# Kernel optimization log

Hardware: AMD Instinct MI355X
Metric: run time of the kernel (lower is better)

The kernel has to match this reference:

```python
import jax, jax.numpy as jnp
import numpy as np

H = 8
D_MODEL = 512
D_K = D_MODEL // H


def setup_inputs() -> dict:
    key = jax.random.key(0)
    ks = jax.random.split(key, 12)
    B, S = 4, 2048
    scale = 1.0 / np.sqrt(D_MODEL)
    inp = {
        "query": jax.random.normal(ks[0], (B, S, D_MODEL), jnp.float32),
        "key": jax.random.normal(ks[1], (B, S, D_MODEL), jnp.float32),
        "value": jax.random.normal(ks[2], (B, S, D_MODEL), jnp.float32),
        "mask": jnp.ones((B, 1, S), jnp.int32),
        "Wq": jax.random.normal(ks[3], (D_MODEL, D_MODEL), jnp.float32) * scale,
        "bq": jax.random.normal(ks[4], (D_MODEL,), jnp.float32) * 0.01,
        "Wk": jax.random.normal(ks[5], (D_MODEL, D_MODEL), jnp.float32) * scale,
        "bk": jax.random.normal(ks[6], (D_MODEL,), jnp.float32) * 0.01,
        "Wv": jax.random.normal(ks[7], (D_MODEL, D_MODEL), jnp.float32) * scale,
        "bv": jax.random.normal(ks[8], (D_MODEL,), jnp.float32) * 0.01,
        "Wo": jax.random.normal(ks[9], (D_MODEL, D_MODEL), jnp.float32) * scale,
        "bo": jax.random.normal(ks[10], (D_MODEL,), jnp.float32) * 0.01,
    }
    return inp


def reference(query, key, value, mask, Wq, bq, Wk, bk, Wv, bv, Wo, bo):
    B, S, _ = query.shape

    def proj(x, W, b):
        # [B,S,D] -> [B,H,S,d_k]
        y = jnp.einsum('bsd,ed->bse', x, W) + b  # torch Linear: x @ W.T + b
        return y.reshape(B, S, H, D_K).transpose(0, 2, 1, 3)

    q = proj(query, Wq, bq)
    k = proj(key, Wk, bk)
    v = proj(value, Wv, bv)

    scores = jnp.einsum('bhqd,bhkd->bhqk', q, k) / jnp.sqrt(jnp.float32(D_K))
    m = mask[:, None, :, :]  # [B,1,1,S]
    scores = jnp.where(m == 0, jnp.float32(-1e9), scores)
    p_attn = jax.nn.softmax(scores, axis=-1)  # dropout is identity in eval
    x = jnp.einsum('bhqk,bhkd->bhqd', p_attn, v)
    x = x.transpose(0, 2, 1, 3).reshape(B, S, D_MODEL)
    return jnp.einsum('bsd,ed->bse', x, Wo) + bo
```

## Files before the change

### kernel.cpp

```cpp
#include <hip/hip_runtime.h>
#include <hip/hip_bf16.h>

#define H 8
#define DMODEL 512
#define DK 64
#define BATCH 4
#define SEQ 2048
#define M_TOTAL (BATCH*SEQ)

typedef short bf16x8 __attribute__((ext_vector_type(8)));
typedef float f32x4 __attribute__((ext_vector_type(4)));
typedef float f32x16 __attribute__((ext_vector_type(16)));

__device__ __forceinline__ unsigned short f2bf(float f) {
    unsigned int u = __builtin_bit_cast(unsigned int, f);
    u += 0x7FFFu + ((u >> 16) & 1u);
    return (unsigned short)(u >> 16);
}

__device__ __forceinline__ unsigned int pack_bf2(float a, float b) {
    unsigned int r;
    asm("v_cvt_pk_bf16_f32 %0, %1, %2" : "=v"(r) : "v"(a), "v"(b));
    return r;
}

__device__ __forceinline__ float exp2_fast(float x) {
    float r;
    asm("v_exp_f32 %0, %1" : "=v"(r) : "v"(x));
    return r;
}

__device__ __forceinline__ f32x16 zero16() {
    f32x16 z;
    #pragma unroll
    for (int i = 0; i < 16; i++) z[i] = 0.f;
    return z;
}

__global__ __launch_bounds__(256) void gemm_qkv(
    const float* __restrict__ query, const float* __restrict__ key_,
    const float* __restrict__ value,
    const float* __restrict__ Wq, const float* __restrict__ bq,
    const float* __restrict__ Wk, const float* __restrict__ bk,
    const float* __restrict__ Wv, const float* __restrict__ bv,
    unsigned short* __restrict__ Qh, unsigned short* __restrict__ Kh,
    unsigned short* __restrict__ Vt)
{
    const int z = blockIdx.z;
    const float* A    = (z == 0) ? query : (z == 1) ? key_ : value;
    const float* W    = (z == 0) ? Wq : (z == 1) ? Wk : Wv;
    const float* bias = (z == 0) ? bq : (z == 1) ? bk : bv;
    unsigned short* out = (z == 0) ? Qh : (z == 1) ? Kh : Vt;

    const int m0 = blockIdx.x * 128;
    const int n0 = blockIdx.y * 64;
    const int tid = threadIdx.x;
    const int lane = tid & 63;
    const int w = tid >> 6;
    const int g = lane >> 4, qi = lane & 15;
    const int wm = w >> 1, wn = w & 1;

    __shared__ unsigned short Alds[128 * 40];
    __shared__ unsigned short Blds[64 * 40];

    f32x4 acc[4][2];
    #pragma unroll
    for (int i = 0; i < 4; i++)
        #pragma unroll
        for (int j = 0; j < 2; j++) acc[i][j] = f32x4{0.f, 0.f, 0.f, 0.f};

    float4 aA[4], bA[2], aB[4], bB[2];

    auto ld = [&](float4 (&ar)[4], float4 (&br)[2], int k0) {
        #pragma unroll
        for (int i = 0; i < 4; i++) { int idx = tid + i * 256;
            ar[i] = *(const float4*)(A + (size_t)(m0 + (idx >> 3)) * 512 + k0 + (idx & 7) * 4); }
        #pragma unroll
        for (int i = 0; i < 2; i++) { int idx = tid + i * 256;
            br[i] = *(const float4*)(W + (size_t)(n0 + (idx >> 3)) * 512 + k0 + (idx & 7) * 4); }
    };
    auto st = [&](float4 (&ar)[4], float4 (&br)[2]) {
        #pragma unroll
        for (int i = 0; i < 4; i++) { int idx = tid + i * 256;
            uint2 p; p.x = pack_bf2(ar[i].x, ar[i].y); p.y = pack_bf2(ar[i].z, ar[i].w);
            *(uint2*)(Alds + (idx >> 3) * 40 + (idx & 7) * 4) = p; }
        #pragma unroll
        for (int i = 0; i < 2; i++) { int idx = tid + i * 256;
            uint2 p; p.x = pack_bf2(br[i].x, br[i].y); p.y = pack_bf2(br[i].z, br[i].w);
            *(uint2*)(Blds + (idx >> 3) * 40 + (idx & 7) * 4) = p; }
    };
    auto tile = [&]() {
        bf16x8 af[4], bf[2];
        #pragma unroll
        for (int mt = 0; mt < 4; mt++)
            af[mt] = *(const bf16x8*)(Alds + (wm * 64 + mt * 16 + qi) * 40 + g * 8);
        #pragma unroll
        for (int nt = 0; nt < 2; nt++)
            bf[nt] = *(const bf16x8*)(Blds + (wn * 32 + nt * 16 + qi) * 40 + g * 8);
        #pragma unroll
        for (int mt = 0; mt < 4; mt++)
            #pragma unroll
            for (int nt = 0; nt < 2; nt++)
                acc[mt][nt] = __builtin_amdgcn_mfma_f32_16x16x32_bf16(af[mt], bf[nt], acc[mt][nt], 0, 0, 0);
    };

    ld(aA, bA, 0);
    for (int k0 = 0; k0 < 512; k0 += 64) {
        __syncthreads();
        st(aA, bA);
        ld(aB, bB, k0 + 32);
        __syncthreads();
        tile();
        __syncthreads();
        st(aB, bB);
        if (k0 + 64 < 512) ld(aA, bA, k0 + 64);
        __syncthreads();
        tile();
    }

    #pragma unroll
    for (int mt = 0; mt < 4; mt++) {
        int mbase = m0 + wm * 64 + mt * 16 + g * 4;
        #pragma unroll
        for (int nt = 0; nt < 2; nt++) {
            int n = n0 + wn * 32 + nt * 16 + qi;
            float bv = bias[n];
            int h = n >> 6, dk = n & 63;
            if (z == 2) {
                int b = mbase >> 11, s = mbase & 2047;
                uint2 pk;
                pk.x = pack_bf2(acc[mt][nt][0] + bv, acc[mt][nt][1] + bv);
                pk.y = pack_bf2(acc[mt][nt][2] + bv, acc[mt][nt][3] + bv);
                *(uint2*)(out + ((size_t)(b * H + h) * 64 + dk) * SEQ + s) = pk;
            } else {
                float sc = (z == 0) ? 0.18033688011112042f : 1.0f;
                #pragma unroll
                for (int r = 0; r < 4; r++) {
                    int m = mbase + r;
                    int b = m >> 11, s = m & 2047;
                    out[((size_t)(b * H + h) * SEQ + s) * 64 + dk] = f2bf((acc[mt][nt][r] + bv) * sc);
                }
            }
        }
    }
}

__global__ __launch_bounds__(256) void gemm_o(
    const unsigned short* __restrict__ Xa, const float* __restrict__ W,
    const float* __restrict__ bias, float* __restrict__ out)
{
    const int m0 = blockIdx.x * 128;
    const int n0 = blockIdx.y * 64;
    const int tid = threadIdx.x;
    const int lane = tid & 63;
    const int w = tid >> 6;
    const int g = lane >> 4, qi = lane & 15;
    const int wm = w >> 1, wn = w & 1;

    __shared__ unsigned short Alds[128 * 40];
    __shared__ unsigned short Blds[64 * 40];

    f32x4 acc[4][2];
    #pragma unroll
    for (int i = 0; i < 4; i++)
        #pragma unroll
        for (int j = 0; j < 2; j++) acc[i][j] = f32x4{0.f, 0.f, 0.f, 0.f};

    bf16x8 aA[2], aB[2];
    float4 bA[2], bB[2];

    auto ld = [&](bf16x8 (&ar)[2], float4 (&br)[2], int k0) {
        #pragma unroll
        for (int i = 0; i < 2; i++) { int idx = tid + i * 256;
            ar[i] = *(const bf16x8*)(Xa + (size_t)(m0 + (idx >> 2)) * 512 + k0 + (idx & 3) * 8); }
        #pragma unroll
        for (int i = 0; i < 2; i++) { int idx = tid + i * 256;
            br[i] = *(const float4*)(W + (size_t)(n0 + (idx >> 3)) * 512 + k0 + (idx & 7) * 4); }
    };
    auto st = [&](bf16x8 (&ar)[2], float4 (&br)[2]) {
        #pragma unroll
        for (int i = 0; i < 2; i++) { int idx = tid + i * 256;
            *(bf16x8*)(Alds + (idx >> 2) * 40 + (idx & 3) * 8) = ar[i]; }
        #pragma unroll
        for (int i = 0; i < 2; i++) { int idx = tid + i * 256;
            uint2 p; p.x = pack_bf2(br[i].x, br[i].y); p.y = pack_bf2(br[i].z, br[i].w);
            *(uint2*)(Blds + (idx >> 3) * 40 + (idx & 7) * 4) = p; }
    };
    auto tile = [&]() {
        bf16x8 af[4], bf[2];
        #pragma unroll
        for (int mt = 0; mt < 4; mt++)
            af[mt] = *(const bf16x8*)(Alds + (wm * 64 + mt * 16 + qi) * 40 + g * 8);
        #pragma unroll
        for (int nt = 0; nt < 2; nt++)
            bf[nt] = *(const bf16x8*)(Blds + (wn * 32 + nt * 16 + qi) * 40 + g * 8);
        #pragma unroll
        for (int mt = 0; mt < 4; mt++)
            #pragma unroll
            for (int nt = 0; nt < 2; nt++)
                acc[mt][nt] = __builtin_amdgcn_mfma_f32_16x16x32_bf16(af[mt], bf[nt], acc[mt][nt], 0, 0, 0);
    };

    ld(aA, bA, 0);
    for (int k0 = 0; k0 < 512; k0 += 64) {
        __syncthreads();
        st(aA, bA);
        ld(aB, bB, k0 + 32);
        __syncthreads();
        tile();
        __syncthreads();
        st(aB, bB);
        if (k0 + 64 < 512) ld(aA, bA, k0 + 64);
        __syncthreads();
        tile();
    }

    #pragma unroll
    for (int mt = 0; mt < 4; mt++) {
        int mbase = m0 + wm * 64 + mt * 16 + g * 4;
        #pragma unroll
        for (int nt = 0; nt < 2; nt++) {
            int n = n0 + wn * 32 + nt * 16 + qi;
            float bv = bias[n];
            #pragma unroll
            for (int r = 0; r < 4; r++)
                out[(size_t)(mbase + r) * 512 + n] = acc[mt][nt][r] + bv;
        }
    }
}

__global__ __launch_bounds__(256, 2) void attn_kernel(
    const unsigned short* __restrict__ Qh,
    const unsigned short* __restrict__ Kh,
    const unsigned short* __restrict__ Vt,
    const int* __restrict__ mask,
    unsigned short* __restrict__ Xattn)
{
    const int tid = threadIdx.x;
    const int lane = tid & 63;
    const int w = tid >> 6;
    const int c = lane & 31;
    const int hi = lane >> 5;
    const int x7 = lane & 7;

    const int bid = blockIdx.x;
    const int xcd = bid & 7;
    const int slot = bid >> 3;
    const int bh = xcd * 4 + (slot >> 4);
    const int q0 = (slot & 15) * 128;
    const int b = bh >> 3;

    __shared__ unsigned short Klds[3][64 * 64];
    __shared__ unsigned short Vlds[3][64 * 64];
    __shared__ int amflag;

    bf16x8 qfr[4];
    {
        const unsigned short* Qbase =
            Qh + ((size_t)bh * SEQ + q0 + w * 32 + c) * 64 + hi * 8;
        #pragma unroll
        for (int seg = 0; seg < 4; seg++)
            qfr[seg] = *(const bf16x8*)(Qbase + seg * 16);
    }

    f32x16 acc[2];
    acc[0] = zero16();
    acc[1] = zero16();
    float l_lane = 0.f;

    const unsigned char* Kbh = (const unsigned char*)(Kh + (size_t)bh * SEQ * 64);
    const unsigned char* Vbh = (const unsigned char*)(Vt + (size_t)bh * 64 * SEQ);
    const int* maskb = mask + b * SEQ;

    if (tid == 0) amflag = 1;
    __syncthreads();
    {
        int v = 1;
        #pragma unroll
        for (int i = 0; i < 8; i++) v &= (maskb[tid + i * 256] != 0) ? 1 : 0;
        if (__ballot(v != 0) != ~0ull && lane == 0) amflag = 0;
    }
    __syncthreads();
    const bool allmask = (amflag != 0);

    const int klane = ((lane >> 3) << 7)  + (((lane & 7) ^ (lane >> 3)) << 4);
    const int vlane = ((lane >> 3) << 12) + (((lane & 7) ^ (lane >> 3)) << 4);

    const int krow = c * 128;

    auto stage = [&](const unsigned char* ks, const unsigned char* vs, int buf) {
        unsigned char* kd = (unsigned char*)&Klds[buf][0];
        unsigned char* vd = (unsigned char*)&Vlds[buf][0];
        #pragma unroll
        for (int j = 0; j < 2; j++) {
            const int cc = w + 4 * j;
            __builtin_amdgcn_global_load_lds(
                (const __attribute__((address_space(1))) unsigned int*)(ks + cc * 1024),
                (__attribute__((address_space(3))) unsigned int*)(kd + cc * 1024), 16, 0, 0);
            __builtin_amdgcn_global_load_lds(
                (const __attribute__((address_space(1))) unsigned int*)(vs + cc * 32768),
                (__attribute__((address_space(3))) unsigned int*)(vd + cc * 1024), 16, 0, 0);
        }
    };

    auto compute = [&](int t, int buf) {
        const unsigned char* KB = (const unsigned char*)&Klds[buf][0];
        const unsigned char* VB = (const unsigned char*)&Vlds[buf][0];
        const int kv0 = t << 6;

        unsigned long long mb = ~0ull;
        if (!allmask) mb = __ballot(maskb[kv0 + lane] != 0);

        #pragma unroll
        for (int kt = 0; kt < 2; kt++) {
            f32x16 sa = zero16();
            __builtin_amdgcn_s_setprio(1);
            #pragma unroll
            for (int seg = 0; seg < 4; seg++) {
                bf16x8 kf = *(const bf16x8*)(
                    KB + kt * 4096 + krow + ((((seg << 1) | hi) ^ x7) << 4));
                sa = __builtin_amdgcn_mfma_f32_32x32x16_bf16(kf, qfr[seg], sa, 0, 0, 0);
            }
            __builtin_amdgcn_s_setprio(0);

            if (mb != ~0ull) {
                #pragma unroll
                for (int r = 0; r < 16; r++) {
                    int kvl = (r & 3) + 8 * (r >> 2) + 4 * hi + 32 * kt;
                    if (!((mb >> kvl) & 1ull)) sa[r] = -1e9f;
                }
            }

            float pe[16];
            #pragma unroll
            for (int r = 0; r < 16; r++) pe[r] = exp2_fast(sa[r]);
            l_lane += (((pe[0] + pe[1]) + (pe[2] + pe[3])) +
                       ((pe[4] + pe[5]) + (pe[6] + pe[7]))) +
                      (((pe[8] + pe[9]) + (pe[10] + pe[11])) +
                       ((pe[12] + pe[13]) + (pe[14] + pe[15])));

            unsigned int a0 = pack_bf2(pe[0],  pe[1]),  a1 = pack_bf2(pe[2],  pe[3]);
            unsigned int b0 = pack_bf2(pe[4],  pe[5]),  b1 = pack_bf2(pe[6],  pe[7]);
            unsigned int c0 = pack_bf2(pe[8],  pe[9]),  c1 = pack_bf2(pe[10], pe[11]);
            unsigned int d0 = pack_bf2(pe[12], pe[13]), d1 = pack_bf2(pe[14], pe[15]);
            asm("v_permlane32_swap_b32 %0, %1" : "+v"(a0), "+v"(b0));
            asm("v_permlane32_swap_b32 %0, %1" : "+v"(a1), "+v"(b1));
            asm("v_permlane32_swap_b32 %0, %1" : "+v"(c0), "+v"(d0));
            asm("v_permlane32_swap_b32 %0, %1" : "+v"(c1), "+v"(d1));
            uint4 u0 = {a0, a1, b0, b1};
            uint4 u1 = {c0, c1, d0, d1};
            bf16x8 pf0 = __builtin_bit_cast(bf16x8, u0);
            bf16x8 pf1 = __builtin_bit_cast(bf16x8, u1);

            __builtin_amdgcn_s_setprio(1);
            #pragma unroll
            for (int dt = 0; dt < 2; dt++) {
                bf16x8 vf0 = *(const bf16x8*)(
                    VB + dt * 4096 + krow + ((((kt << 2) | 0 | hi) ^ x7) << 4));
                acc[dt] = __builtin_amdgcn_mfma_f32_32x32x16_bf16(vf0, pf0, acc[dt], 0, 0, 0);
                bf16x8 vf1 = *(const bf16x8*)(
                    VB + dt * 4096 + krow + ((((kt << 2) | 2 | hi) ^ x7) << 4));
                acc[dt] = __builtin_amdgcn_mfma_f32_32x32x16_bf16(vf1, pf1, acc[dt], 0, 0, 0);
            }
            __builtin_amdgcn_s_setprio(0);
        }
    };

    const unsigned char* ks = Kbh + klane;
    const unsigned char* vs = Vbh + vlane;

    stage(ks, vs, 0); ks += 8192; vs += 128;
    stage(ks, vs, 1); ks += 8192; vs += 128;
    int bc = 0, bs = 2;
    #pragma unroll 1
    for (int t = 0; t < 32; ++t) {
        if (t < 31) __builtin_amdgcn_s_waitcnt(0xF74);
        else        __builtin_amdgcn_s_waitcnt(0xF70);
        __builtin_amdgcn_s_barrier();
        compute(t, bc);
        if (t + 2 < 32) {
            stage(ks, vs, bs);
            ks += 8192; vs += 128;
        }
        bc = (bc == 2) ? 0 : bc + 1;
        bs = (bs == 2) ? 0 : bs + 1;
    }

    const int h = bh & 7;
    float l = l_lane + __shfl_xor(l_lane, 32);
    const float inv = 1.0f / l;
    const int s = q0 + w * 32 + c;
    size_t base = ((size_t)b * SEQ + s) * 512 + h * 64;
    #pragma unroll
    for (int dt = 0; dt < 2; dt++) {
        #pragma unroll
        for (int rg = 0; rg < 4; rg++) {
            const int d0i = rg * 8 + hi * 4 + dt * 32;
            uint2 o;
            o.x = pack_bf2(acc[dt][4 * rg]     * inv, acc[dt][4 * rg + 1] * inv);
            o.y = pack_bf2(acc[dt][4 * rg + 2] * inv, acc[dt][4 * rg + 3] * inv);
            *(uint2*)(Xattn + base + d0i) = o;
        }
    }
}

extern "C" void kernel_launch(void* const* d_in, const int* in_sizes, int n_in,
                              void* d_out, int out_size, void* d_ws, size_t ws_size,
                              hipStream_t stream)
{
    const float* query = (const float*)d_in[0];
    const float* key_  = (const float*)d_in[1];
    const float* value = (const float*)d_in[2];
    const int*   mask  = (const int*)d_in[3];
    const float* Wq = (const float*)d_in[4];
    const float* bq = (const float*)d_in[5];
    const float* Wk = (const float*)d_in[6];
    const float* bk = (const float*)d_in[7];
    const float* Wv = (const float*)d_in[8];
    const float* bv = (const float*)d_in[9];
    const float* Wo = (const float*)d_in[10];
    const float* bo = (const float*)d_in[11];

    unsigned short* Qh = (unsigned short*)d_ws;
    unsigned short* Kh = Qh + (size_t)M_TOTAL * DMODEL;
    unsigned short* Vt = Kh + (size_t)M_TOTAL * DMODEL;
    unsigned short* Xa = Vt + (size_t)M_TOTAL * DMODEL;

    hipLaunchKernelGGL(gemm_qkv, dim3(64, 8, 3), dim3(256), 0, stream,
                       query, key_, value, Wq, bq, Wk, bk, Wv, bv, Qh, Kh, Vt);
    hipLaunchKernelGGL(attn_kernel, dim3(512), dim3(256), 0, stream, Qh, Kh, Vt, mask, Xa);
    hipLaunchKernelGGL(gemm_o, dim3(64, 8), dim3(256), 0, stream, Xa, Wo, bo, (float*)d_out);
}
```

Before: 89.92 us.

## Software-pipeline QK^T of next tile with softmax/PV of previous tile

Restructures the attention loop so each iteration issues the QK^T MFMAs for the current KV tile and then runs exp/pack/PV for the previous tile, letting the two stages overlap. The LDS ring grows from three to four buffers so the previous tile's V stays valid while new tiles are staged. The two score MFMA chains are interleaved to expose more independent work. This raises register pressure and LDS use and adds an epilogue.

```diff
diff --git a/kernel.cpp b/kernel.cpp
--- a/kernel.cpp
+++ b/kernel.cpp
@@ -250,8 +250,8 @@
     const int q0 = (slot & 15) * 128;
     const int b = bh >> 3;
 
-    __shared__ unsigned short Klds[3][64 * 64];
-    __shared__ unsigned short Vlds[3][64 * 64];
+    __shared__ unsigned short Klds[4][64 * 64];
+    __shared__ unsigned short Vlds[4][64 * 64];
     __shared__ int amflag;
 
     bf16x8 qfr[4];
@@ -303,26 +303,11 @@
         }
     };
 
-    auto compute = [&](int t, int buf) {
-        const unsigned char* KB = (const unsigned char*)&Klds[buf][0];
-        const unsigned char* VB = (const unsigned char*)&Vlds[buf][0];
-        const int kv0 = t << 6;
-
-        unsigned long long mb = ~0ull;
-        if (!allmask) mb = __ballot(maskb[kv0 + lane] != 0);
-
+    auto sm_pv = [&](f32x16& s0, f32x16& s1, const unsigned char* VB,
+                     unsigned long long mb) {
         #pragma unroll
         for (int kt = 0; kt < 2; kt++) {
-            f32x16 sa = zero16();
-            __builtin_amdgcn_s_setprio(1);
-            #pragma unroll
-            for (int seg = 0; seg < 4; seg++) {
-                bf16x8 kf = *(const bf16x8*)(
-                    KB + kt * 4096 + krow + ((((seg << 1) | hi) ^ x7) << 4));
-                sa = __builtin_amdgcn_mfma_f32_32x32x16_bf16(kf, qfr[seg], sa, 0, 0, 0);
-            }
-            __builtin_amdgcn_s_setprio(0);
-
+            f32x16& sa = kt ? s1 : s0;
             if (mb != ~0ull) {
                 #pragma unroll
                 for (int r = 0; r < 16; r++) {
@@ -330,7 +315,6 @@
                     if (!((mb >> kvl) & 1ull)) sa[r] = -1e9f;
                 }
             }
-
             float pe[16];
             #pragma unroll
             for (int r = 0; r < 16; r++) pe[r] = exp2_fast(sa[r]);
@@ -371,20 +355,40 @@
 
     stage(ks, vs, 0); ks += 8192; vs += 128;
     stage(ks, vs, 1); ks += 8192; vs += 128;
-    int bc = 0, bs = 2;
+
+    f32x16 saP0, saP1;
+    unsigned long long mbP = ~0ull;
     #pragma unroll 1
     for (int t = 0; t < 32; ++t) {
         if (t < 31) __builtin_amdgcn_s_waitcnt(0xF74);
         else        __builtin_amdgcn_s_waitcnt(0xF70);
         __builtin_amdgcn_s_barrier();
-        compute(t, bc);
         if (t + 2 < 32) {
-            stage(ks, vs, bs);
+            stage(ks, vs, (t + 2) & 3);
             ks += 8192; vs += 128;
         }
-        bc = (bc == 2) ? 0 : bc + 1;
-        bs = (bs == 2) ? 0 : bs + 1;
-    }
+
+        const unsigned char* KB = (const unsigned char*)&Klds[t & 3][0];
+        unsigned long long mbC = ~0ull;
+        if (!allmask) mbC = __ballot(maskb[(t << 6) + lane] != 0);
+        f32x16 sc0 = zero16(), sc1 = zero16();
+        __builtin_amdgcn_s_setprio(1);
+        #pragma unroll
+        for (int seg = 0; seg < 4; seg++) {
+            const int so = (((seg << 1) | hi) ^ x7) << 4;
+            bf16x8 kf0 = *(const bf16x8*)(KB + krow + so);
+            sc0 = __builtin_amdgcn_mfma_f32_32x32x16_bf16(kf0, qfr[seg], sc0, 0, 0, 0);
+            bf16x8 kf1 = *(const bf16x8*)(KB + 4096 + krow + so);
+            sc1 = __builtin_amdgcn_mfma_f32_32x32x16_bf16(kf1, qfr[seg], sc1, 0, 0, 0);
+        }
+        __builtin_amdgcn_s_setprio(0);
+
+        if (t > 0)
+            sm_pv(saP0, saP1, (const unsigned char*)&Vlds[(t - 1) & 3][0], mbP);
+
+        saP0 = sc0; saP1 = sc1; mbP = mbC;
+    }
+    sm_pv(saP0, saP1, (const unsigned char*)&Vlds[31 & 3][0], mbP);
 
     const int h = bh & 7;
     float l = l_lane + __shfl_xor(l_lane, 32);
```

Result: slower. 92.40 us (+2.8%).

## Enlarge QKV GEMM tile to 256x64 and drop register double-buffering

Applied to the files above, without the earlier changes.

The QKV projection GEMM block tile grows from 128x64 to 256x64, with each wave owning a 64x64 sub-tile instead of 64x32. This raises reuse of the loaded W tile and halves the grid size. The register-prefetch double-buffered pipeline is replaced by a simple load-convert-store then compute loop per 32-wide K step, which exposes global load latency and lowers occupancy from more LDS and registers. The grid shrinks to 768 blocks.

```diff
diff --git a/kernel.cpp b/kernel.cpp
--- a/kernel.cpp
+++ b/kernel.cpp
@@ -52,78 +52,60 @@
     const float* bias = (z == 0) ? bq : (z == 1) ? bk : bv;
     unsigned short* out = (z == 0) ? Qh : (z == 1) ? Kh : Vt;
 
-    const int m0 = blockIdx.x * 128;
+    const int m0 = blockIdx.x * 256;
     const int n0 = blockIdx.y * 64;
     const int tid = threadIdx.x;
     const int lane = tid & 63;
     const int w = tid >> 6;
     const int g = lane >> 4, qi = lane & 15;
-    const int wm = w >> 1, wn = w & 1;
-
-    __shared__ unsigned short Alds[128 * 40];
+
+    __shared__ unsigned short Alds[256 * 40];
     __shared__ unsigned short Blds[64 * 40];
 
-    f32x4 acc[4][2];
+    f32x4 acc[4][4];
     #pragma unroll
     for (int i = 0; i < 4; i++)
         #pragma unroll
-        for (int j = 0; j < 2; j++) acc[i][j] = f32x4{0.f, 0.f, 0.f, 0.f};
-
-    float4 aA[4], bA[2], aB[4], bB[2];
-
-    auto ld = [&](float4 (&ar)[4], float4 (&br)[2], int k0) {
-        #pragma unroll
-        for (int i = 0; i < 4; i++) { int idx = tid + i * 256;
-            ar[i] = *(const float4*)(A + (size_t)(m0 + (idx >> 3)) * 512 + k0 + (idx & 7) * 4); }
-        #pragma unroll
-        for (int i = 0; i < 2; i++) { int idx = tid + i * 256;
-            br[i] = *(const float4*)(W + (size_t)(n0 + (idx >> 3)) * 512 + k0 + (idx & 7) * 4); }
-    };
-    auto st = [&](float4 (&ar)[4], float4 (&br)[2]) {
-        #pragma unroll
-        for (int i = 0; i < 4; i++) { int idx = tid + i * 256;
-            uint2 p; p.x = pack_bf2(ar[i].x, ar[i].y); p.y = pack_bf2(ar[i].z, ar[i].w);
-            *(uint2*)(Alds + (idx >> 3) * 40 + (idx & 7) * 4) = p; }
-        #pragma unroll
-        for (int i = 0; i < 2; i++) { int idx = tid + i * 256;
-            uint2 p; p.x = pack_bf2(br[i].x, br[i].y); p.y = pack_bf2(br[i].z, br[i].w);
-            *(uint2*)(Blds + (idx >> 3) * 40 + (idx & 7) * 4) = p; }
-    };
-    auto tile = [&]() {
-        bf16x8 af[4], bf[2];
+        for (int j = 0; j < 4; j++) acc[i][j] = f32x4{0.f, 0.f, 0.f, 0.f};
+
+    for (int k0 = 0; k0 < 512; k0 += 32) {
+        __syncthreads();
+        #pragma unroll
+        for (int i = 0; i < 8; i++) {
+            int idx = tid + i * 256;
+            float4 v = *(const float4*)(A + (size_t)(m0 + (idx >> 3)) * 512 + k0 + (idx & 7) * 4);
+            uint2 p; p.x = pack_bf2(v.x, v.y); p.y = pack_bf2(v.z, v.w);
+            *(uint2*)(Alds + (idx >> 3) * 40 + (idx & 7) * 4) = p;
+        }
+        #pragma unroll
+        for (int i = 0; i < 2; i++) {
+            int idx = tid + i * 256;
+            float4 v = *(const float4*)(W + (size_t)(n0 + (idx >> 3)) * 512 + k0 + (idx & 7) * 4);
+            uint2 p; p.x = pack_bf2(v.x, v.y); p.y = pack_bf2(v.z, v.w);
+            *(uint2*)(Blds + (idx >> 3) * 40 + (idx & 7) * 4) = p;
+        }
+        __syncthreads();
+
+        bf16x8 af[4], bf[4];
         #pragma unroll
         for (int mt = 0; mt < 4; mt++)
-            af[mt] = *(const bf16x8*)(Alds + (wm * 64 + mt * 16 + qi) * 40 + g * 8);
-        #pragma unroll
-        for (int nt = 0; nt < 2; nt++)
-            bf[nt] = *(const bf16x8*)(Blds + (wn * 32 + nt * 16 + qi) * 40 + g * 8);
+            af[mt] = *(const bf16x8*)(Alds + (w * 64 + mt * 16 + qi) * 40 + g * 8);
+        #pragma unroll
+        for (int nt = 0; nt < 4; nt++)
+            bf[nt] = *(const bf16x8*)(Blds + (nt * 16 + qi) * 40 + g * 8);
         #pragma unroll
         for (int mt = 0; mt < 4; mt++)
             #pragma unroll
-            for (int nt = 0; nt < 2; nt++)
+            for (int nt = 0; nt < 4; nt++)
                 acc[mt][nt] = __builtin_amdgcn_mfma_f32_16x16x32_bf16(af[mt], bf[nt], acc[mt][nt], 0, 0, 0);
-    };
-
-    ld(aA, bA, 0);
-    for (int k0 = 0; k0 < 512; k0 += 64) {
-        __syncthreads();
-        st(aA, bA);
-        ld(aB, bB, k0 + 32);
-        __syncthreads();
-        tile();
-        __syncthreads();
-        st(aB, bB);
-        if (k0 + 64 < 512) ld(aA, bA, k0 + 64);
-        __syncthreads();
-        tile();
     }
 
     #pragma unroll
     for (int mt = 0; mt < 4; mt++) {
-        int mbase = m0 + wm * 64 + mt * 16 + g * 4;
-        #pragma unroll
-        for (int nt = 0; nt < 2; nt++) {
-            int n = n0 + wn * 32 + nt * 16 + qi;
+        int mbase = m0 + w * 64 + mt * 16 + g * 4;
+        #pragma unroll
+        for (int nt = 0; nt < 4; nt++) {
+            int n = n0 + nt * 16 + qi;
             float bv = bias[n];
             int h = n >> 6, dk = n & 63;
             if (z == 2) {
@@ -426,7 +408,7 @@
     unsigned short* Vt = Kh + (size_t)M_TOTAL * DMODEL;
     unsigned short* Xa = Vt + (size_t)M_TOTAL * DMODEL;
 
-    hipLaunchKernelGGL(gemm_qkv, dim3(64, 8, 3), dim3(256), 0, stream,
+    hipLaunchKernelGGL(gemm_qkv, dim3(32, 8, 3), dim3(256), 0, stream,
                        query, key_, value, Wq, bq, Wk, bk, Wv, bv, Qh, Kh, Vt);
     hipLaunchKernelGGL(attn_kernel, dim3(512), dim3(256), 0, stream, Qh, Kh, Vt, mask, Xa);
     hipLaunchKernelGGL(gemm_o, dim3(64, 8), dim3(256), 0, stream, Xa, Wo, bo, (float*)d_out);
```

Result: no change. 89.83 us (-0.1%).

## Interleave both KV subtiles with split PV accumulators and issue prefetch before compute

Applied to the files above, without the earlier changes.

Processes the two 32-row key subtiles of each 64-key tile together: both QK MFMA chains are interleaved, then softmax exp for both, then PV MFMAs go into two separate accumulator sets (A/B) that are summed at the end. This breaks the serial dependency on a single accumulator and gives the scheduler independent MFMA chains to overlap. The next tile's global-to-LDS prefetch is now issued before compute instead of after, so loads start earlier. It raises register pressure through the extra accumulators and live exp values, which can cut occupancy, and issuing the prefetch early depends on the 3-buffer rotation keeping the staged buffer distinct from the one being read.

```diff
diff --git a/kernel.cpp b/kernel.cpp
--- a/kernel.cpp
+++ b/kernel.cpp
@@ -263,9 +263,9 @@
             qfr[seg] = *(const bf16x8*)(Qbase + seg * 16);
     }
 
-    f32x16 acc[2];
-    acc[0] = zero16();
-    acc[1] = zero16();
+    f32x16 accA[2], accB[2];
+    accA[0] = zero16(); accA[1] = zero16();
+    accB[0] = zero16(); accB[1] = zero16();
     float l_lane = 0.f;
 
     const unsigned char* Kbh = (const unsigned char*)(Kh + (size_t)bh * SEQ * 64);
@@ -311,59 +311,75 @@
         unsigned long long mb = ~0ull;
         if (!allmask) mb = __ballot(maskb[kv0 + lane] != 0);
 
-        #pragma unroll
-        for (int kt = 0; kt < 2; kt++) {
-            f32x16 sa = zero16();
-            __builtin_amdgcn_s_setprio(1);
+        f32x16 sa0 = zero16(), sa1 = zero16();
+        __builtin_amdgcn_s_setprio(1);
+        #pragma unroll
+        for (int seg = 0; seg < 4; seg++) {
+            const int so = (((seg << 1) | hi) ^ x7) << 4;
+            bf16x8 kf0 = *(const bf16x8*)(KB + krow + so);
+            sa0 = __builtin_amdgcn_mfma_f32_32x32x16_bf16(kf0, qfr[seg], sa0, 0, 0, 0);
+            bf16x8 kf1 = *(const bf16x8*)(KB + 4096 + krow + so);
+            sa1 = __builtin_amdgcn_mfma_f32_32x32x16_bf16(kf1, qfr[seg], sa1, 0, 0, 0);
+        }
+        __builtin_amdgcn_s_setprio(0);
+
+        if (mb != ~0ull) {
             #pragma unroll
-            for (int seg = 0; seg < 4; seg++) {
-                bf16x8 kf = *(const bf16x8*)(
-                    KB + kt * 4096 + krow + ((((seg << 1) | hi) ^ x7) << 4));
-                sa = __builtin_amdgcn_mfma_f32_32x32x16_bf16(kf, qfr[seg], sa, 0, 0, 0);
+            for (int r = 0; r < 16; r++) {
+                int kvl = (r & 3) + 8 * (r >> 2) + 4 * hi;
+                if (!((mb >> kvl) & 1ull)) sa0[r] = -1e9f;
+                if (!((mb >> (kvl + 32)) & 1ull)) sa1[r] = -1e9f;
             }
-            __builtin_amdgcn_s_setprio(0);
-
-            if (mb != ~0ull) {
-                #pragma unroll
-                for (int r = 0; r < 16; r++) {
-                    int kvl = (r & 3) + 8 * (r >> 2) + 4 * hi + 32 * kt;
-                    if (!((mb >> kvl) & 1ull)) sa[r] = -1e9f;
-                }
-            }
-
-            float pe[16];
-            #pragma unroll
-            for (int r = 0; r < 16; r++) pe[r] = exp2_fast(sa[r]);
-            l_lane += (((pe[0] + pe[1]) + (pe[2] + pe[3])) +
-                       ((pe[4] + pe[5]) + (pe[6] + pe[7]))) +
-                      (((pe[8] + pe[9]) + (pe[10] + pe[11])) +
-                       ((pe[12] + pe[13]) + (pe[14] + pe[15])));
-
-            unsigned int a0 = pack_bf2(pe[0],  pe[1]),  a1 = pack_bf2(pe[2],  pe[3]);
-            unsigned int b0 = pack_bf2(pe[4],  pe[5]),  b1 = pack_bf2(pe[6],  pe[7]);
-            unsigned int c0 = pack_bf2(pe[8],  pe[9]),  c1 = pack_bf2(pe[10], pe[11]);
-            unsigned int d0 = pack_bf2(pe[12], pe[13]), d1 = pack_bf2(pe[14], pe[15]);
-            asm("v_permlane32_swap_b32 %0, %1" : "+v"(a0), "+v"(b0));
-            asm("v_permlane32_swap_b32 %0, %1" : "+v"(a1), "+v"(b1));
-            asm("v_permlane32_swap_b32 %0, %1" : "+v"(c0), "+v"(d0));
-            asm("v_permlane32_swap_b32 %0, %1" : "+v"(c1), "+v"(d1));
-            uint4 u0 = {a0, a1, b0, b1};
-            uint4 u1 = {c0, c1, d0, d1};
-            bf16x8 pf0 = __builtin_bit_cast(bf16x8, u0);
-            bf16x8 pf1 = __builtin_bit_cast(bf16x8, u1);
-
-            __builtin_amdgcn_s_setprio(1);
-            #pragma unroll
-            for (int dt = 0; dt < 2; dt++) {
-                bf16x8 vf0 = *(const bf16x8*)(
-                    VB + dt * 4096 + krow + ((((kt << 2) | 0 | hi) ^ x7) << 4));
-                acc[dt] = __builtin_amdgcn_mfma_f32_32x32x16_bf16(vf0, pf0, acc[dt], 0, 0, 0);
-                bf16x8 vf1 = *(const bf16x8*)(
-                    VB + dt * 4096 + krow + ((((kt << 2) | 2 | hi) ^ x7) << 4));
-                acc[dt] = __builtin_amdgcn_mfma_f32_32x32x16_bf16(vf1, pf1, acc[dt], 0, 0, 0);
-            }
-            __builtin_amdgcn_s_setprio(0);
-        }
+        }
+
+        float pe0[16], pe1[16];
+        #pragma unroll
+        for (int r = 0; r < 16; r++) pe0[r] = exp2_fast(sa0[r]);
+        #pragma unroll
+        for (int r = 0; r < 16; r++) pe1[r] = exp2_fast(sa1[r]);
+        float s0 = 0.f, s1 = 0.f;
+        #pragma unroll
+        for (int r = 0; r < 16; r++) { s0 += pe0[r]; s1 += pe1[r]; }
+        l_lane += s0 + s1;
+
+        unsigned int a0 = pack_bf2(pe0[0],  pe0[1]),  a1 = pack_bf2(pe0[2],  pe0[3]);
+        unsigned int b0 = pack_bf2(pe0[4],  pe0[5]),  b1 = pack_bf2(pe0[6],  pe0[7]);
+        unsigned int c0 = pack_bf2(pe0[8],  pe0[9]),  c1 = pack_bf2(pe0[10], pe0[11]);
+        unsigned int d0 = pack_bf2(pe0[12], pe0[13]), d1 = pack_bf2(pe0[14], pe0[15]);
+        asm("v_permlane32_swap_b32 %0, %1" : "+v"(a0), "+v"(b0));
+        asm("v_permlane32_swap_b32 %0, %1" : "+v"(a1), "+v"(b1));
+        asm("v_permlane32_swap_b32 %0, %1" : "+v"(c0), "+v"(d0));
+        asm("v_permlane32_swap_b32 %0, %1" : "+v"(c1), "+v"(d1));
+        unsigned int e0 = pack_bf2(pe1[0],  pe1[1]),  e1 = pack_bf2(pe1[2],  pe1[3]);
+        unsigned int f0 = pack_bf2(pe1[4],  pe1[5]),  f1 = pack_bf2(pe1[6],  pe1[7]);
+        unsigned int g0 = pack_bf2(pe1[8],  pe1[9]),  g1 = pack_bf2(pe1[10], pe1[11]);
+        unsigned int h0 = pack_bf2(pe1[12], pe1[13]), h1 = pack_bf2(pe1[14], pe1[15]);
+        asm("v_permlane32_swap_b32 %0, %1" : "+v"(e0), "+v"(f0));
+        asm("v_permlane32_swap_b32 %0, %1" : "+v"(e1), "+v"(f1));
+        asm("v_permlane32_swap_b32 %0, %1" : "+v"(g0), "+v"(h0));
+        asm("v_permlane32_swap_b32 %0, %1" : "+v"(g1), "+v"(h1));
+        uint4 u00 = {a0, a1, b0, b1};
+        uint4 u01 = {c0, c1, d0, d1};
+        uint4 u10 = {e0, e1, f0, f1};
+        uint4 u11 = {g0, g1, h0, h1};
+        bf16x8 pf00 = __builtin_bit_cast(bf16x8, u00);
+        bf16x8 pf01 = __builtin_bit_cast(bf16x8, u01);
+        bf16x8 pf10 = __builtin_bit_cast(bf16x8, u10);
+        bf16x8 pf11 = __builtin_bit_cast(bf16x8, u11);
+
+        __builtin_amdgcn_s_setprio(1);
+        #pragma unroll
+        for (int dt = 0; dt < 2; dt++) {
+            bf16x8 va0 = *(const bf16x8*)(VB + dt * 4096 + krow + (((0 | hi) ^ x7) << 4));
+            accA[dt] = __builtin_amdgcn_mfma_f32_32x32x16_bf16(va0, pf00, accA[dt], 0, 0, 0);
+            bf16x8 vb0 = *(const bf16x8*)(VB + dt * 4096 + krow + (((4 | hi) ^ x7) << 4));
+            accB[dt] = __builtin_amdgcn_mfma_f32_32x32x16_bf16(vb0, pf10, accB[dt], 0, 0, 0);
+            bf16x8 va1 = *(const bf16x8*)(VB + dt * 4096 + krow + (((2 | hi) ^ x7) << 4));
+            accA[dt] = __builtin_amdgcn_mfma_f32_32x32x16_bf16(va1, pf01, accA[dt], 0, 0, 0);
+            bf16x8 vb1 = *(const bf16x8*)(VB + dt * 4096 + krow + (((6 | hi) ^ x7) << 4));
+            accB[dt] = __builtin_amdgcn_mfma_f32_32x32x16_bf16(vb1, pf11, accB[dt], 0, 0, 0);
+        }
+        __builtin_amdgcn_s_setprio(0);
     };
 
     const unsigned char* ks = Kbh + klane;
@@ -377,11 +393,11 @@
         if (t < 31) __builtin_amdgcn_s_waitcnt(0xF74);
         else        __builtin_amdgcn_s_waitcnt(0xF70);
         __builtin_amdgcn_s_barrier();
-        compute(t, bc);
         if (t + 2 < 32) {
             stage(ks, vs, bs);
             ks += 8192; vs += 128;
         }
+        compute(t, bc);
         bc = (bc == 2) ? 0 : bc + 1;
         bs = (bs == 2) ? 0 : bs + 1;
     }
@@ -397,8 +413,10 @@
         for (int rg = 0; rg < 4; rg++) {
             const int d0i = rg * 8 + hi * 4 + dt * 32;
             uint2 o;
-            o.x = pack_bf2(acc[dt][4 * rg]     * inv, acc[dt][4 * rg + 1] * inv);
-            o.y = pack_bf2(acc[dt][4 * rg + 2] * inv, acc[dt][4 * rg + 3] * inv);
+            o.x = pack_bf2((accA[dt][4 * rg]     + accB[dt][4 * rg])     * inv,
+                           (accA[dt][4 * rg + 1] + accB[dt][4 * rg + 1]) * inv);
+            o.y = pack_bf2((accA[dt][4 * rg + 2] + accB[dt][4 * rg + 2]) * inv,
+                           (accA[dt][4 * rg + 3] + accB[dt][4 * rg + 3]) * inv);
             *(uint2*)(Xattn + base + d0i) = o;
         }
     }
```

Measured after the change: 93.35 us. +3.8%, slower.
